# Kernel optimization log

Measured on AMD Instinct MI355X. Metric: run time of the kernel, lower is better.

The kernel has to match this reference:

```python
import jax, jax.numpy as jnp
import numpy as np

EPS = 1e-5

def _layernorm(x, w, b):
    mu = jnp.mean(x, axis=-1, keepdims=True)
    var = jnp.mean(jnp.square(x - mu), axis=-1, keepdims=True)
    return (x - mu) * jax.lax.rsqrt(var + EPS) * w + b

def setup_inputs() -> dict:
    key = jax.random.key(0)
    ks = jax.random.split(key, 8)
    B, N, D = 1, 512, 128
    x = jax.random.normal(ks[0], (B, N, N, D), dtype=jnp.float32)
    mask = jnp.ones((B, N, N), dtype=jnp.float32)
    # learned params (torch nn.Linear stores weight as (out, in))
    p_in_w = jax.random.normal(ks[1], (2 * D, D), dtype=jnp.float32) * (1.0 / np.sqrt(D))
    g_in_w = jax.random.normal(ks[2], (2 * D, D), dtype=jnp.float32) * 0.02
    p_out_w = jax.random.normal(ks[3], (D, D), dtype=jnp.float32) * 0.02
    g_out_w = jax.random.normal(ks[4], (D, D), dtype=jnp.float32) * 0.02
    norm_in_w = jnp.ones((D,), dtype=jnp.float32)
    norm_in_b = jnp.zeros((D,), dtype=jnp.float32)
    norm_out_w = jnp.ones((D,), dtype=jnp.float32)
    norm_out_b = jnp.zeros((D,), dtype=jnp.float32)
    return {"x": x, "mask": mask, "norm_in_w": norm_in_w, "norm_in_b": norm_in_b,
            "p_in_w": p_in_w, "g_in_w": g_in_w, "norm_out_w": norm_out_w,
            "norm_out_b": norm_out_b, "p_out_w": p_out_w, "g_out_w": g_out_w}

def reference(x, mask, norm_in_w, norm_in_b, p_in_w, g_in_w, norm_out_w, norm_out_b, p_out_w, g_out_w):
    # x: (B,N,N,D), mask: (B,N,N)
    x_ln = _layernorm(x, norm_in_w, norm_in_b)          # (B,N,N,D)
    x_in = x_ln
    # gated dual projection to 2D channels, then mask
    h = jnp.einsum('bijd,ed->bije', x_ln, p_in_w) * jax.nn.sigmoid(
        jnp.einsum('bijd,ed->bije', x_ln, g_in_w))      # (B,N,N,2D)
    h = h * mask[..., None]
    D = x.shape[-1]
    a, b = h[..., :D], h[..., D:]                        # (B,N,N,D) each
    # triangular 'outgoing' contraction over k
    t = jnp.einsum('bikd,bjkd->bijd', a, b)              # (B,N,N,D)
    out = jnp.einsum('bijd,ed->bije', _layernorm(t, norm_out_w, norm_out_b), p_out_w) \
        * jax.nn.sigmoid(jnp.einsum('bijd,ed->bije', x_in, g_out_w))
    return out
```

## Files before the change

kernel.cpp:

```cpp
#include <hip/hip_runtime.h>
#include <stdint.h>

#define NSEQ 512
#define DDIM 128
#define NROWS (NSEQ * NSEQ)
#define PMASK (NROWS - 1)
#define ROT(idx, d) (((idx) + (d) * 128) & PMASK)

typedef __bf16 bf16x8 __attribute__((ext_vector_type(8)));
typedef __bf16 bf16x2v __attribute__((ext_vector_type(2)));
typedef unsigned short u16;
typedef u16 ushort8 __attribute__((ext_vector_type(8)));
typedef float f32x4 __attribute__((ext_vector_type(4)));
typedef uint32_t u32x4 __attribute__((ext_vector_type(4)));
typedef uint32_t u32x2 __attribute__((ext_vector_type(2)));

__device__ __forceinline__ u16 cvt1(float f) {
  return __builtin_bit_cast(u16, (__bf16)f);
}
__device__ __forceinline__ uint32_t pk2(float a, float b) {
  bf16x2v v = {(__bf16)a, (__bf16)b};
  return __builtin_bit_cast(uint32_t, v);
}
__device__ __forceinline__ float bf2f(u16 u) {
  uint32_t x = ((uint32_t)u) << 16;
  return __builtin_bit_cast(float, x);
}
__device__ __forceinline__ f32x4 mfma_bf16(ushort8 a, ushort8 b, f32x4 c) {
  return __builtin_amdgcn_mfma_f32_16x16x32_bf16(
      __builtin_bit_cast(bf16x8, a), __builtin_bit_cast(bf16x8, b), c, 0, 0, 0);
}
__device__ __forceinline__ float sigmoidf_(float x) {
  return __builtin_amdgcn_rcpf(1.0f + __expf(-x));
}

#define ROR16(v, n)                                                            \
  __builtin_bit_cast(float, __builtin_amdgcn_update_dpp(                       \
      __builtin_bit_cast(int, (v)), __builtin_bit_cast(int, (v)),              \
      0x120 + (n), 0xF, 0xF, false))

#define GLOAD16(gp, lp)                                                        \
  __builtin_amdgcn_global_load_lds(                                            \
      (const __attribute__((address_space(1))) void*)(gp),                     \
      (__attribute__((address_space(3))) void*)(lp), 16, 0, 0)

__global__ __launch_bounds__(256) void k0_prep(
    const float* __restrict__ p_in_w, const float* __restrict__ g_in_w,
    const float* __restrict__ p_out_w, const float* __restrict__ g_out_w,
    const float* __restrict__ now, const float* __restrict__ nob,
    u16* __restrict__ Wb, u16* __restrict__ Pb, u16* __restrict__ Gb,
    float* __restrict__ S12) {
  const int b = blockIdx.x, t = threadIdx.x;
#pragma unroll
  for (int k = 0; k < 2; ++k) {
    const int idx = b * 512 + k * 256 + t;
    const float v = (idx < 32768) ? p_in_w[idx] : g_in_w[idx - 32768];
    Wb[idx] = cvt1(v);
  }
  if (t < 128) {
    const int idx = b * 128 + t;
    const int d = idx & 127;
    Pb[idx] = cvt1(p_out_w[idx] * now[d]);
    Gb[idx] = cvt1(g_out_w[idx]);
  }
  const int w = t >> 6, lane = t & 63;
  if (w >= 2) {
    const float* wv = (w == 2) ? now : nob;
    float p = p_out_w[b * 128 + lane] * wv[lane] +
              p_out_w[b * 128 + 64 + lane] * wv[64 + lane];
#pragma unroll
    for (int m = 1; m < 64; m <<= 1) p += __shfl_xor(p, m);
    if (lane == 0) S12[2 * b + (w - 2)] = p;
  }
}

__global__ __launch_bounds__(256, 6) void k1_ln_proj(
    const float* __restrict__ x, const float* __restrict__ mask,
    const float* __restrict__ niw, const float* __restrict__ nib,
    const u16* __restrict__ Wb, const u16* __restrict__ Gb,
    u16* __restrict__ AtB, u16* __restrict__ gArg) {
  __shared__ __align__(16) u16 xln[64 * 128];
  __shared__ __align__(16) u16 stage[64 * 64];
  const int tid = threadIdx.x;
  const int lane = tid & 63;
  const int w = tid >> 6;
  const int bid = blockIdx.x;
  const int rb = (bid >> 5) * 8 + (bid & 7);
  const int cg = (bid >> 3) & 3;
  const int r0 = rb * 64;
  const int g = lane >> 4, c = lane & 15;

  f32x4 v0[4], v1[4];
#pragma unroll
  for (int it = 0; it < 4; ++it) {
    const int rl = w * 16 + it * 4 + g;
    const float* xr = x + (size_t)(r0 + rl) * DDIM + c * 8;
    v0[it] = *(const f32x4*)xr;
    v1[it] = *(const f32x4*)(xr + 4);
  }
  const f32x4 w0 = *(const f32x4*)(niw + c * 8);
  const f32x4 w1 = *(const f32x4*)(niw + c * 8 + 4);
  const f32x4 b0 = *(const f32x4*)(nib + c * 8);
  const f32x4 b1 = *(const f32x4*)(nib + c * 8 + 4);
#pragma unroll
  for (int it = 0; it < 4; ++it) {
    const int rl = w * 16 + it * 4 + g;
    float s = v0[it][0] + v0[it][1] + v0[it][2] + v0[it][3] +
              v1[it][0] + v1[it][1] + v1[it][2] + v1[it][3];
    float ss = v0[it][0] * v0[it][0] + v0[it][1] * v0[it][1] +
               v0[it][2] * v0[it][2] + v0[it][3] * v0[it][3] +
               v1[it][0] * v1[it][0] + v1[it][1] * v1[it][1] +
               v1[it][2] * v1[it][2] + v1[it][3] * v1[it][3];
    { float t1 = ROR16(s, 1); s += t1; t1 = ROR16(ss, 1); ss += t1; }
    { float t1 = ROR16(s, 2); s += t1; t1 = ROR16(ss, 2); ss += t1; }
    { float t1 = ROR16(s, 4); s += t1; t1 = ROR16(ss, 4); ss += t1; }
    { float t1 = ROR16(s, 8); s += t1; t1 = ROR16(ss, 8); ss += t1; }
    const float mu = s * (1.0f / 128.0f);
    const float rs = rsqrtf(ss * (1.0f / 128.0f) - mu * mu + 1e-5f);
    float f0 = (v0[it][0] - mu) * rs * w0[0] + b0[0];
    float f1 = (v0[it][1] - mu) * rs * w0[1] + b0[1];
    float f2 = (v0[it][2] - mu) * rs * w0[2] + b0[2];
    float f3 = (v0[it][3] - mu) * rs * w0[3] + b0[3];
    float f4 = (v1[it][0] - mu) * rs * w1[0] + b1[0];
    float f5 = (v1[it][1] - mu) * rs * w1[1] + b1[1];
    float f6 = (v1[it][2] - mu) * rs * w1[2] + b1[2];
    float f7 = (v1[it][3] - mu) * rs * w1[3] + b1[3];
    u32x4 ov{pk2(f0, f1), pk2(f2, f3), pk2(f4, f5), pk2(f6, f7)};
    const int byteoff = rl * 256 + ((c ^ (rl & 7)) << 4);
    *(u32x4*)((char*)xln + byteoff) = ov;
  }
  __syncthreads();

  const int lr = lane & 15, lq = lane >> 4;
  const int eP = cg * 64 + w * 16;
  f32x4 accP[4], accG[4];
#pragma unroll
  for (int m = 0; m < 4; ++m) {
    accP[m] = f32x4{0.f, 0.f, 0.f, 0.f};
    accG[m] = f32x4{0.f, 0.f, 0.f, 0.f};
  }

#pragma unroll
  for (int ks = 0; ks < 4; ++ks) {
    const int kblk = ks * 4 + lq;
    ushort8 af[4];
#pragma unroll
    for (int m = 0; m < 4; ++m) {
      const int row = m * 16 + lr;
      af[m] = *(const ushort8*)((const char*)xln + row * 256 +
                                ((kblk ^ (row & 7)) << 4));
    }
    const int e = eP + lr;
    const int dd = ks * 32 + lq * 8;
    const ushort8 bP = *(const ushort8*)(Wb + e * 128 + dd);
    const ushort8 bG = *(const ushort8*)(Wb + (256 + e) * 128 + dd);
#pragma unroll
    for (int m = 0; m < 4; ++m) {
      accP[m] = mfma_bf16(af[m], bP, accP[m]);
      accG[m] = mfma_bf16(af[m], bG, accG[m]);
    }
  }

  const int dloc = w * 16 + lr;
#pragma unroll
  for (int m = 0; m < 4; ++m) {
    const int rloc = m * 16 + lq * 4;
    const f32x4 mv = *(const f32x4*)(mask + r0 + rloc);
    const float o0 = accP[m][0] * sigmoidf_(accG[m][0]) * mv[0];
    const float o1 = accP[m][1] * sigmoidf_(accG[m][1]) * mv[1];
    const float o2 = accP[m][2] * sigmoidf_(accG[m][2]) * mv[2];
    const float o3 = accP[m][3] * sigmoidf_(accG[m][3]) * mv[3];
    u32x2 pk;
    pk[0] = pk2(o0, o1);
    pk[1] = pk2(o2, o3);
    const int gsw = (m * 4 + lq) ^ (dloc & 15);
    *(u32x2*)((char*)stage + dloc * 128 + (gsw << 3)) = pk;
  }
  __syncthreads();

  {
    const int i_ = rb >> 3, kt = rb & 7;
    u16* dst = AtB + (((size_t)kt * 512 + i_) * 256 + cg * 64) * 64;
#pragma unroll
    for (int q = 0; q < 2; ++q) {
      const int e = q * 32 + (tid >> 3);
      const int g0 = (tid & 7) * 2;
      const u32x2 lo =
          *(const u32x2*)((const char*)stage + e * 128 + ((g0 ^ (e & 15)) << 3));
      const u32x2 hi = *(const u32x2*)((const char*)stage + e * 128 +
                                       (((g0 + 1) ^ (e & 15)) << 3));
      u32x4 outv{lo[0], lo[1], hi[0], hi[1]};
      *(u32x4*)(dst + e * 64 + (tid & 7) * 8) = outv;
    }
  }

  if (cg < 2) {
    f32x4 accO[4];
#pragma unroll
    for (int m = 0; m < 4; ++m) accO[m] = f32x4{0.f, 0.f, 0.f, 0.f};
    const int eg = cg * 64 + w * 16 + lr;
#pragma unroll
    for (int ks = 0; ks < 4; ++ks) {
      const int kblk = ks * 4 + lq;
      const ushort8 bO = *(const ushort8*)(Gb + eg * 128 + ks * 32 + lq * 8);
#pragma unroll
      for (int m = 0; m < 4; ++m) {
        const int row = m * 16 + lr;
        const ushort8 af2 = *(const ushort8*)((const char*)xln + row * 256 +
                                              ((kblk ^ (row & 7)) << 4));
        accO[m] = mfma_bf16(af2, bO, accO[m]);
      }
    }
    __syncthreads();
    u16* stage2 = stage;
    const int e_loc = w * 16 + lr;
    const int gsl = e_loc >> 2;
    const int esub = (e_loc & 3) * 2;
#pragma unroll
    for (int m = 0; m < 4; ++m) {
#pragma unroll
      for (int reg = 0; reg < 4; ++reg) {
        const int rl2 = m * 16 + lq * 4 + reg;
        *(u16*)((char*)stage2 + rl2 * 128 + ((gsl ^ (rl2 & 7)) << 3) + esub) =
            cvt1(accO[m][reg]);
      }
    }
    __syncthreads();
#pragma unroll
    for (int p = 0; p < 2; ++p) {
      const int r = p * 32 + (tid >> 3);
      const int il8 = tid & 7;
      const char* base = (const char*)stage2 + r * 128;
      const u32x2 a = *(const u32x2*)(base + (((il8 * 2) ^ (r & 7)) << 3));
      const u32x2 b = *(const u32x2*)(base + (((il8 * 2 + 1) ^ (r & 7)) << 3));
      u32x4 ov{a[0], a[1], b[0], b[1]};
      *(u32x4*)(gArg + (size_t)(r0 + r) * DDIM + cg * 64 + il8 * 8) = ov;
    }
  }
}

__global__ __launch_bounds__(256, 4) void k2_tri(const u16* __restrict__ AtB,
                                                 u16* __restrict__ Ct) {
  __shared__ __align__(16) u16 lds[16384];
  const int tid = threadIdx.x;
  const int bid = blockIdx.x;
  const int lb = (bid & 7) * 256 + (bid >> 3);
  const int d = lb >> 4;
  const int tile = lb & 15;
  const int i0 = (tile >> 2) * 128, j0 = (tile & 3) * 128;
  const int lane = tid & 63, wid = tid >> 6;
  const int wr = wid >> 1, wc = wid & 1;
  const int lr = lane & 15, lq = lane >> 4;

  f32x4 acc[4][4];
#pragma unroll
  for (int m = 0; m < 4; ++m)
#pragma unroll
    for (int n = 0; n < 4; ++n) acc[m][n] = f32x4{0.f, 0.f, 0.f, 0.f};

  for (int kt = 0; kt < 8; ++kt) {
    if (kt) __syncthreads();
#pragma unroll
    for (int q = 0; q < 4; ++q) {
      const int idx = q * 256 + tid;
      const int r = idx >> 3, bk = idx & 7;
      const int sbk = bk ^ (r & 7);
      GLOAD16(AtB + (((size_t)kt * 512 + i0 + r) * 256 + d) * 64 + sbk * 8,
              &lds[idx * 8]);
      GLOAD16(AtB + (((size_t)kt * 512 + j0 + r) * 256 + 128 + d) * 64 + sbk * 8,
              &lds[8192 + idx * 8]);
    }
    __syncthreads();

    const u16* A_l = lds;
    const u16* B_l = lds + 8192;
#pragma unroll
    for (int ks = 0; ks < 2; ++ks) {
      const int kblk = ks * 4 + lq;
      ushort8 af[4], bfr[4];
#pragma unroll
      for (int m = 0; m < 4; ++m) {
        const int row = wr * 64 + m * 16 + lr;
        af[m] = *(const ushort8*)((const char*)A_l + row * 128 +
                                  ((kblk ^ (row & 7)) << 4));
      }
#pragma unroll
      for (int n = 0; n < 4; ++n) {
        const int col = wc * 64 + n * 16 + lr;
        bfr[n] = *(const ushort8*)((const char*)B_l + col * 128 +
                                   ((kblk ^ (col & 7)) << 4));
      }
#pragma unroll
      for (int m = 0; m < 4; ++m)
#pragma unroll
        for (int n = 0; n < 4; ++n)
          acc[m][n] = mfma_bf16(af[m], bfr[n], acc[m][n]);
    }
  }

  u16* Cd = Ct + (size_t)d * NROWS;
#pragma unroll
  for (int m = 0; m < 4; ++m) {
    const int i = i0 + wr * 64 + m * 16 + lq * 4;
#pragma unroll
    for (int n = 0; n < 4; ++n) {
      const int j = j0 + wc * 64 + n * 16 + lr;
#pragma unroll
      for (int reg = 0; reg < 4; ++reg)
        Cd[ROT((i + reg) * NSEQ + j, d)] = cvt1(acc[m][n][reg]);
    }
  }
}

__global__ __launch_bounds__(256, 4) void k3_out(
    const u16* __restrict__ Ct, const u16* __restrict__ gArg,
    const u16* __restrict__ Pb, const float* __restrict__ S12,
    float* __restrict__ out) {
  __shared__ __align__(16) u16 ldsT[128 * 128];
  __shared__ float ps[4 * 128], pss[4 * 128];
  __shared__ float prm[128 * 2];
  __shared__ float s12l[128 * 2];
  const int tid = threadIdx.x, lane = tid & 63, w = tid >> 6;
  const int c0 = blockIdx.x * 128;

  {
    const int row2 = lane * 2;
    float s0 = 0.f, ss0 = 0.f, s1 = 0.f, ss1 = 0.f;
#pragma unroll
    for (int db = 0; db < 4; ++db) {
      uint32_t pe[4], po[4];
#pragma unroll
      for (int j = 0; j < 8; ++j) {
        const int d = w * 32 + db * 8 + j;
        const uint32_t v = *(const uint32_t*)(Ct + (size_t)d * NROWS +
                                              ROT(c0 + row2, d));
        const u16 ue = (u16)v, uo = (u16)(v >> 16);
        const float fe = bf2f(ue), fo = bf2f(uo);
        s0 += fe; ss0 += fe * fe;
        s1 += fo; ss1 += fo * fo;
        if (j & 1) {
          pe[j >> 1] |= ((uint32_t)ue) << 16;
          po[j >> 1] |= ((uint32_t)uo) << 16;
        } else {
          pe[j >> 1] = ue;
          po[j >> 1] = uo;
        }
      }
      const int gr = w * 4 + db;
      *(u32x4*)((char*)ldsT + row2 * 256 + ((gr ^ (row2 & 7)) << 4)) =
          u32x4{pe[0], pe[1], pe[2], pe[3]};
      *(u32x4*)((char*)ldsT + (row2 + 1) * 256 + ((gr ^ ((row2 + 1) & 7)) << 4)) =
          u32x4{po[0], po[1], po[2], po[3]};
    }
    ps[w * 128 + row2] = s0;
    pss[w * 128 + row2] = ss0;
    ps[w * 128 + row2 + 1] = s1;
    pss[w * 128 + row2 + 1] = ss1;
  }
  if (tid < 128) ((u32x2*)s12l)[tid] = ((const u32x2*)S12)[tid];
  __syncthreads();
  if (tid < 128) {
    const float s = ps[tid] + ps[128 + tid] + ps[256 + tid] + ps[384 + tid];
    const float ss = pss[tid] + pss[128 + tid] + pss[256 + tid] + pss[384 + tid];
    const float mu = s * (1.f / 128.f);
    const float rs = rsqrtf(ss * (1.f / 128.f) - mu * mu + 1e-5f);
    prm[2 * tid] = rs;
    prm[2 * tid + 1] = -rs * mu;
  }

  const int lr = lane & 15, lq = lane >> 4;
  const int rowbase = w * 32;
  f32x4 aP[2][8];
#pragma unroll
  for (int m = 0; m < 2; ++m)
#pragma unroll
    for (int n = 0; n < 8; ++n) aP[m][n] = f32x4{0.f, 0.f, 0.f, 0.f};
#pragma unroll
  for (int ks = 0; ks < 4; ++ks) {
    const int kblk = ks * 4 + lq;
    ushort8 at2[2];
#pragma unroll
    for (int m = 0; m < 2; ++m) {
      const int row = rowbase + m * 16 + lr;
      at2[m] = *(const ushort8*)((const char*)ldsT + row * 256 +
                                 ((kblk ^ (row & 7)) << 4));
    }
    ushort8 bp[8];
#pragma unroll
    for (int n = 0; n < 8; ++n) {
      const int e = n * 16 + lr;
      bp[n] = *(const ushort8*)(Pb + e * 128 + ks * 32 + lq * 8);
    }
#pragma unroll
    for (int m = 0; m < 2; ++m)
#pragma unroll
      for (int n = 0; n < 8; ++n) aP[m][n] = mfma_bf16(at2[m], bp[n], aP[m][n]);
  }
  __syncthreads();

#pragma unroll
  for (int m = 0; m < 2; ++m) {
    const int crow = rowbase + m * 16 + lq * 4;
#pragma unroll
    for (int n = 0; n < 8; ++n) {
      const int e = n * 16 + lr;
      const float s1 = s12l[2 * e], s2v = s12l[2 * e + 1];
#pragma unroll
      for (int reg = 0; reg < 4; ++reg) {
        const float rs = prm[2 * (crow + reg)];
        const float t1 = prm[2 * (crow + reg) + 1];
        const float op = rs * aP[m][n][reg] + t1 * s1 + s2v;
        const size_t r = (size_t)(c0 + crow + reg);
        const float gt = sigmoidf_(bf2f(gArg[r * DDIM + e]));
        out[r * DDIM + e] = op * gt;
      }
    }
  }
}

extern "C" void kernel_launch(void* const* d_in, const int* in_sizes, int n_in,
                              void* d_out, int out_size, void* d_ws,
                              size_t ws_size, hipStream_t stream) {
  const float* x = (const float*)d_in[0];
  const float* mask = (const float*)d_in[1];
  const float* niw = (const float*)d_in[2];
  const float* nib = (const float*)d_in[3];
  const float* p_in_w = (const float*)d_in[4];
  const float* g_in_w = (const float*)d_in[5];
  const float* now = (const float*)d_in[6];
  const float* nob = (const float*)d_in[7];
  const float* p_out_w = (const float*)d_in[8];
  const float* g_out_w = (const float*)d_in[9];
  float* out = (float*)d_out;
  char* ws = (char*)d_ws;

  u16* AtB = (u16*)(ws);
  u16* Ct = (u16*)(ws + 134217728);
  u16* gA = (u16*)(ws + 201326592);
  u16* Wb = (u16*)(ws + 268435456);
  u16* Pb = (u16*)(ws + 268566528);
  u16* Gb = (u16*)(ws + 268599296);
  float* S12 = (float*)(ws + 268632064);

  hipLaunchKernelGGL(k0_prep, dim3(128), dim3(256), 0, stream, p_in_w, g_in_w,
                     p_out_w, g_out_w, now, nob, Wb, Pb, Gb, S12);
  hipLaunchKernelGGL(k1_ln_proj, dim3(4 * NROWS / 64), dim3(256), 0, stream, x,
                     mask, niw, nib, Wb, Gb, AtB, gA);
  hipLaunchKernelGGL(k2_tri, dim3(128 * 16), dim3(256), 0, stream, AtB, Ct);
  hipLaunchKernelGGL(k3_out, dim3(NROWS / 128), dim3(256), 0, stream, Ct, gA,
                     Pb, S12, out);
}
```

Baseline: 322.1 us.

## Make LN-projection blocks loop over four row tiles with register prefetch

The layernorm and input-projection kernel now launches a quarter as many blocks. Each block processes four 64-row tiles in sequence, keeping the same channel group and XCD mapping. While the MFMA projections and stores for the current tile run, the next tile's x rows are loaded into registers, so global-load latency overlaps with compute. The cost is more live registers per thread and less parallelism from independent blocks, and correctness now depends on the barrier placement that guards the reused LDS buffers.

```diff
diff --git a/kernel.cpp b/kernel.cpp
--- a/kernel.cpp
+++ b/kernel.cpp
@@ -85,156 +85,176 @@
   const int lane = tid & 63;
   const int w = tid >> 6;
   const int bid = blockIdx.x;
-  const int rb = (bid >> 5) * 8 + (bid & 7);
+  const int xcd = bid & 7;
   const int cg = (bid >> 3) & 3;
-  const int r0 = rb * 64;
+  const int ub = bid >> 5;
   const int g = lane >> 4, c = lane & 15;
-
-  f32x4 v0[4], v1[4];
-#pragma unroll
-  for (int it = 0; it < 4; ++it) {
-    const int rl = w * 16 + it * 4 + g;
-    const float* xr = x + (size_t)(r0 + rl) * DDIM + c * 8;
-    v0[it] = *(const f32x4*)xr;
-    v1[it] = *(const f32x4*)(xr + 4);
-  }
+  const int lr = lane & 15, lq = lane >> 4;
+
   const f32x4 w0 = *(const f32x4*)(niw + c * 8);
   const f32x4 w1 = *(const f32x4*)(niw + c * 8 + 4);
   const f32x4 b0 = *(const f32x4*)(nib + c * 8);
   const f32x4 b1 = *(const f32x4*)(nib + c * 8 + 4);
-#pragma unroll
+
+  f32x4 v0[4], v1[4];
+  {
+    const int r0n = ((ub * 4 + 0) * 8 + xcd) * 64;
+#pragma unroll
+    for (int itl = 0; itl < 4; ++itl) {
+      const int rl = w * 16 + itl * 4 + g;
+      const float* xr = x + (size_t)(r0n + rl) * DDIM + c * 8;
+      v0[itl] = *(const f32x4*)xr;
+      v1[itl] = *(const f32x4*)(xr + 4);
+    }
+  }
+
   for (int it = 0; it < 4; ++it) {
-    const int rl = w * 16 + it * 4 + g;
-    float s = v0[it][0] + v0[it][1] + v0[it][2] + v0[it][3] +
-              v1[it][0] + v1[it][1] + v1[it][2] + v1[it][3];
-    float ss = v0[it][0] * v0[it][0] + v0[it][1] * v0[it][1] +
-               v0[it][2] * v0[it][2] + v0[it][3] * v0[it][3] +
-               v1[it][0] * v1[it][0] + v1[it][1] * v1[it][1] +
-               v1[it][2] * v1[it][2] + v1[it][3] * v1[it][3];
-    { float t1 = ROR16(s, 1); s += t1; t1 = ROR16(ss, 1); ss += t1; }
-    { float t1 = ROR16(s, 2); s += t1; t1 = ROR16(ss, 2); ss += t1; }
-    { float t1 = ROR16(s, 4); s += t1; t1 = ROR16(ss, 4); ss += t1; }
-    { float t1 = ROR16(s, 8); s += t1; t1 = ROR16(ss, 8); ss += t1; }
-    const float mu = s * (1.0f / 128.0f);
-    const float rs = rsqrtf(ss * (1.0f / 128.0f) - mu * mu + 1e-5f);
-    float f0 = (v0[it][0] - mu) * rs * w0[0] + b0[0];
-    float f1 = (v0[it][1] - mu) * rs * w0[1] + b0[1];
-    float f2 = (v0[it][2] - mu) * rs * w0[2] + b0[2];
-    float f3 = (v0[it][3] - mu) * rs * w0[3] + b0[3];
-    float f4 = (v1[it][0] - mu) * rs * w1[0] + b1[0];
-    float f5 = (v1[it][1] - mu) * rs * w1[1] + b1[1];
-    float f6 = (v1[it][2] - mu) * rs * w1[2] + b1[2];
-    float f7 = (v1[it][3] - mu) * rs * w1[3] + b1[3];
-    u32x4 ov{pk2(f0, f1), pk2(f2, f3), pk2(f4, f5), pk2(f6, f7)};
-    const int byteoff = rl * 256 + ((c ^ (rl & 7)) << 4);
-    *(u32x4*)((char*)xln + byteoff) = ov;
-  }
-  __syncthreads();
-
-  const int lr = lane & 15, lq = lane >> 4;
-  const int eP = cg * 64 + w * 16;
-  f32x4 accP[4], accG[4];
-#pragma unroll
-  for (int m = 0; m < 4; ++m) {
-    accP[m] = f32x4{0.f, 0.f, 0.f, 0.f};
-    accG[m] = f32x4{0.f, 0.f, 0.f, 0.f};
-  }
-
-#pragma unroll
-  for (int ks = 0; ks < 4; ++ks) {
-    const int kblk = ks * 4 + lq;
-    ushort8 af[4];
+    const int rb = (ub * 4 + it) * 8 + xcd;
+    const int r0 = rb * 64;
+
+#pragma unroll
+    for (int itl = 0; itl < 4; ++itl) {
+      const int rl = w * 16 + itl * 4 + g;
+      float s = v0[itl][0] + v0[itl][1] + v0[itl][2] + v0[itl][3] +
+                v1[itl][0] + v1[itl][1] + v1[itl][2] + v1[itl][3];
+      float ss = v0[itl][0] * v0[itl][0] + v0[itl][1] * v0[itl][1] +
+                 v0[itl][2] * v0[itl][2] + v0[itl][3] * v0[itl][3] +
+                 v1[itl][0] * v1[itl][0] + v1[itl][1] * v1[itl][1] +
+                 v1[itl][2] * v1[itl][2] + v1[itl][3] * v1[itl][3];
+      { float t1 = ROR16(s, 1); s += t1; t1 = ROR16(ss, 1); ss += t1; }
+      { float t1 = ROR16(s, 2); s += t1; t1 = ROR16(ss, 2); ss += t1; }
+      { float t1 = ROR16(s, 4); s += t1; t1 = ROR16(ss, 4); ss += t1; }
+      { float t1 = ROR16(s, 8); s += t1; t1 = ROR16(ss, 8); ss += t1; }
+      const float mu = s * (1.0f / 128.0f);
+      const float rs = rsqrtf(ss * (1.0f / 128.0f) - mu * mu + 1e-5f);
+      const float f0 = (v0[itl][0] - mu) * rs * w0[0] + b0[0];
+      const float f1 = (v0[itl][1] - mu) * rs * w0[1] + b0[1];
+      const float f2 = (v0[itl][2] - mu) * rs * w0[2] + b0[2];
+      const float f3 = (v0[itl][3] - mu) * rs * w0[3] + b0[3];
+      const float f4 = (v1[itl][0] - mu) * rs * w1[0] + b1[0];
+      const float f5 = (v1[itl][1] - mu) * rs * w1[1] + b1[1];
+      const float f6 = (v1[itl][2] - mu) * rs * w1[2] + b1[2];
+      const float f7 = (v1[itl][3] - mu) * rs * w1[3] + b1[3];
+      u32x4 ov{pk2(f0, f1), pk2(f2, f3), pk2(f4, f5), pk2(f6, f7)};
+      const int byteoff = rl * 256 + ((c ^ (rl & 7)) << 4);
+      *(u32x4*)((char*)xln + byteoff) = ov;
+    }
+    __syncthreads();
+
+    if (it < 3) {
+      const int r0n = ((ub * 4 + it + 1) * 8 + xcd) * 64;
+#pragma unroll
+      for (int itl = 0; itl < 4; ++itl) {
+        const int rl = w * 16 + itl * 4 + g;
+        const float* xr = x + (size_t)(r0n + rl) * DDIM + c * 8;
+        v0[itl] = *(const f32x4*)xr;
+        v1[itl] = *(const f32x4*)(xr + 4);
+      }
+    }
+
+    const int eP = cg * 64 + w * 16;
+    f32x4 accP[4], accG[4];
 #pragma unroll
     for (int m = 0; m < 4; ++m) {
-      const int row = m * 16 + lr;
-      af[m] = *(const ushort8*)((const char*)xln + row * 256 +
-                                ((kblk ^ (row & 7)) << 4));
-    }
-    const int e = eP + lr;
-    const int dd = ks * 32 + lq * 8;
-    const ushort8 bP = *(const ushort8*)(Wb + e * 128 + dd);
-    const ushort8 bG = *(const ushort8*)(Wb + (256 + e) * 128 + dd);
-#pragma unroll
-    for (int m = 0; m < 4; ++m) {
-      accP[m] = mfma_bf16(af[m], bP, accP[m]);
-      accG[m] = mfma_bf16(af[m], bG, accG[m]);
-    }
-  }
-
-  const int dloc = w * 16 + lr;
-#pragma unroll
-  for (int m = 0; m < 4; ++m) {
-    const int rloc = m * 16 + lq * 4;
-    const f32x4 mv = *(const f32x4*)(mask + r0 + rloc);
-    const float o0 = accP[m][0] * sigmoidf_(accG[m][0]) * mv[0];
-    const float o1 = accP[m][1] * sigmoidf_(accG[m][1]) * mv[1];
-    const float o2 = accP[m][2] * sigmoidf_(accG[m][2]) * mv[2];
-    const float o3 = accP[m][3] * sigmoidf_(accG[m][3]) * mv[3];
-    u32x2 pk;
-    pk[0] = pk2(o0, o1);
-    pk[1] = pk2(o2, o3);
-    const int gsw = (m * 4 + lq) ^ (dloc & 15);
-    *(u32x2*)((char*)stage + dloc * 128 + (gsw << 3)) = pk;
-  }
-  __syncthreads();
-
-  {
-    const int i_ = rb >> 3, kt = rb & 7;
-    u16* dst = AtB + (((size_t)kt * 512 + i_) * 256 + cg * 64) * 64;
-#pragma unroll
-    for (int q = 0; q < 2; ++q) {
-      const int e = q * 32 + (tid >> 3);
-      const int g0 = (tid & 7) * 2;
-      const u32x2 lo =
-          *(const u32x2*)((const char*)stage + e * 128 + ((g0 ^ (e & 15)) << 3));
-      const u32x2 hi = *(const u32x2*)((const char*)stage + e * 128 +
-                                       (((g0 + 1) ^ (e & 15)) << 3));
-      u32x4 outv{lo[0], lo[1], hi[0], hi[1]};
-      *(u32x4*)(dst + e * 64 + (tid & 7) * 8) = outv;
-    }
-  }
-
-  if (cg < 2) {
-    f32x4 accO[4];
-#pragma unroll
-    for (int m = 0; m < 4; ++m) accO[m] = f32x4{0.f, 0.f, 0.f, 0.f};
-    const int eg = cg * 64 + w * 16 + lr;
+      accP[m] = f32x4{0.f, 0.f, 0.f, 0.f};
+      accG[m] = f32x4{0.f, 0.f, 0.f, 0.f};
+    }
 #pragma unroll
     for (int ks = 0; ks < 4; ++ks) {
       const int kblk = ks * 4 + lq;
-      const ushort8 bO = *(const ushort8*)(Gb + eg * 128 + ks * 32 + lq * 8);
+      ushort8 af[4];
 #pragma unroll
       for (int m = 0; m < 4; ++m) {
         const int row = m * 16 + lr;
-        const ushort8 af2 = *(const ushort8*)((const char*)xln + row * 256 +
-                                              ((kblk ^ (row & 7)) << 4));
-        accO[m] = mfma_bf16(af2, bO, accO[m]);
-      }
+        af[m] = *(const ushort8*)((const char*)xln + row * 256 +
+                                  ((kblk ^ (row & 7)) << 4));
+      }
+      const int e = eP + lr;
+      const int dd = ks * 32 + lq * 8;
+      const ushort8 bP = *(const ushort8*)(Wb + e * 128 + dd);
+      const ushort8 bG = *(const ushort8*)(Wb + (256 + e) * 128 + dd);
+#pragma unroll
+      for (int m = 0; m < 4; ++m) {
+        accP[m] = mfma_bf16(af[m], bP, accP[m]);
+        accG[m] = mfma_bf16(af[m], bG, accG[m]);
+      }
+    }
+
+    const int dloc = w * 16 + lr;
+#pragma unroll
+    for (int m = 0; m < 4; ++m) {
+      const int rloc = m * 16 + lq * 4;
+      const f32x4 mv = *(const f32x4*)(mask + r0 + rloc);
+      const float o0 = accP[m][0] * sigmoidf_(accG[m][0]) * mv[0];
+      const float o1 = accP[m][1] * sigmoidf_(accG[m][1]) * mv[1];
+      const float o2 = accP[m][2] * sigmoidf_(accG[m][2]) * mv[2];
+      const float o3 = accP[m][3] * sigmoidf_(accG[m][3]) * mv[3];
+      u32x2 pk;
+      pk[0] = pk2(o0, o1);
+      pk[1] = pk2(o2, o3);
+      const int gsw = (m * 4 + lq) ^ (dloc & 15);
+      *(u32x2*)((char*)stage + dloc * 128 + (gsw << 3)) = pk;
     }
     __syncthreads();
-    u16* stage2 = stage;
-    const int e_loc = w * 16 + lr;
-    const int gsl = e_loc >> 2;
-    const int esub = (e_loc & 3) * 2;
-#pragma unroll
-    for (int m = 0; m < 4; ++m) {
-#pragma unroll
-      for (int reg = 0; reg < 4; ++reg) {
-        const int rl2 = m * 16 + lq * 4 + reg;
-        *(u16*)((char*)stage2 + rl2 * 128 + ((gsl ^ (rl2 & 7)) << 3) + esub) =
-            cvt1(accO[m][reg]);
-      }
-    }
-    __syncthreads();
-#pragma unroll
-    for (int p = 0; p < 2; ++p) {
-      const int r = p * 32 + (tid >> 3);
-      const int il8 = tid & 7;
-      const char* base = (const char*)stage2 + r * 128;
-      const u32x2 a = *(const u32x2*)(base + (((il8 * 2) ^ (r & 7)) << 3));
-      const u32x2 b = *(const u32x2*)(base + (((il8 * 2 + 1) ^ (r & 7)) << 3));
-      u32x4 ov{a[0], a[1], b[0], b[1]};
-      *(u32x4*)(gArg + (size_t)(r0 + r) * DDIM + cg * 64 + il8 * 8) = ov;
+
+    {
+      const int i_ = rb >> 3, kt = rb & 7;
+      u16* dst = AtB + (((size_t)kt * 512 + i_) * 256 + cg * 64) * 64;
+#pragma unroll
+      for (int q = 0; q < 2; ++q) {
+        const int e = q * 32 + (tid >> 3);
+        const int g0 = (tid & 7) * 2;
+        const u32x2 lo = *(const u32x2*)((const char*)stage + e * 128 +
+                                         ((g0 ^ (e & 15)) << 3));
+        const u32x2 hi = *(const u32x2*)((const char*)stage + e * 128 +
+                                         (((g0 + 1) ^ (e & 15)) << 3));
+        u32x4 outv{lo[0], lo[1], hi[0], hi[1]};
+        *(u32x4*)(dst + e * 64 + (tid & 7) * 8) = outv;
+      }
+    }
+
+    if (cg < 2) {
+      f32x4 accO[4];
+#pragma unroll
+      for (int m = 0; m < 4; ++m) accO[m] = f32x4{0.f, 0.f, 0.f, 0.f};
+      const int eg = cg * 64 + w * 16 + lr;
+#pragma unroll
+      for (int ks = 0; ks < 4; ++ks) {
+        const int kblk = ks * 4 + lq;
+        const ushort8 bO = *(const ushort8*)(Gb + eg * 128 + ks * 32 + lq * 8);
+#pragma unroll
+        for (int m = 0; m < 4; ++m) {
+          const int row = m * 16 + lr;
+          const ushort8 af2 = *(const ushort8*)((const char*)xln + row * 256 +
+                                                ((kblk ^ (row & 7)) << 4));
+          accO[m] = mfma_bf16(af2, bO, accO[m]);
+        }
+      }
+      __syncthreads();
+      u16* stage2 = stage;
+      const int e_loc = w * 16 + lr;
+      const int gsl = e_loc >> 2;
+      const int esub = (e_loc & 3) * 2;
+#pragma unroll
+      for (int m = 0; m < 4; ++m) {
+#pragma unroll
+        for (int reg = 0; reg < 4; ++reg) {
+          const int rl2 = m * 16 + lq * 4 + reg;
+          *(u16*)((char*)stage2 + rl2 * 128 + ((gsl ^ (rl2 & 7)) << 3) + esub) =
+              cvt1(accO[m][reg]);
+        }
+      }
+      __syncthreads();
+#pragma unroll
+      for (int p = 0; p < 2; ++p) {
+        const int r = p * 32 + (tid >> 3);
+        const int il8 = tid & 7;
+        const char* base = (const char*)stage2 + r * 128;
+        const u32x2 a = *(const u32x2*)(base + (((il8 * 2) ^ (r & 7)) << 3));
+        const u32x2 b = *(const u32x2*)(base + (((il8 * 2 + 1) ^ (r & 7)) << 3));
+        u32x4 ov{a[0], a[1], b[0], b[1]};
+        *(u32x4*)(gArg + (size_t)(r0 + r) * DDIM + cg * 64 + il8 * 8) = ov;
+      }
     }
   }
 }
@@ -444,8 +464,8 @@
 
   hipLaunchKernelGGL(k0_prep, dim3(128), dim3(256), 0, stream, p_in_w, g_in_w,
                      p_out_w, g_out_w, now, nob, Wb, Pb, Gb, S12);
-  hipLaunchKernelGGL(k1_ln_proj, dim3(4 * NROWS / 64), dim3(256), 0, stream, x,
-                     mask, niw, nib, Wb, Gb, AtB, gA);
+  hipLaunchKernelGGL(k1_ln_proj, dim3(4096), dim3(256), 0, stream, x, mask,
+                     niw, nib, Wb, Gb, AtB, gA);
   hipLaunchKernelGGL(k2_tri, dim3(128 * 16), dim3(256), 0, stream, AtB, Ct);
   hipLaunchKernelGGL(k3_out, dim3(NROWS / 128), dim3(256), 0, stream, Ct, gA,
                      Pb, S12, out);
```

New measurement: 637.5 us. 98.0% more time.

## Halve k1 column groups so each block computes 128 output channels

Applied to the files above, without the earlier changes.

The LN+projection kernel now splits the 256 gated channels across 2 column groups instead of 4, with each wave computing two 16-wide channel tiles. Each 64-row tile of x is therefore loaded and layer-normalized twice instead of four times, cutting redundant global reads and LN work. The gate-out projection now runs in every block. The cost is more accumulator registers and a larger staging buffer, so launch bounds drop to 4 blocks per SM and occupancy may fall.

```diff
diff --git a/kernel.cpp b/kernel.cpp
--- a/kernel.cpp
+++ b/kernel.cpp
@@ -74,19 +74,19 @@
   }
 }
 
-__global__ __launch_bounds__(256, 6) void k1_ln_proj(
+__global__ __launch_bounds__(256, 4) void k1_ln_proj(
     const float* __restrict__ x, const float* __restrict__ mask,
     const float* __restrict__ niw, const float* __restrict__ nib,
     const u16* __restrict__ Wb, const u16* __restrict__ Gb,
     u16* __restrict__ AtB, u16* __restrict__ gArg) {
   __shared__ __align__(16) u16 xln[64 * 128];
-  __shared__ __align__(16) u16 stage[64 * 64];
+  __shared__ __align__(16) u16 stage[128 * 64];
   const int tid = threadIdx.x;
   const int lane = tid & 63;
   const int w = tid >> 6;
   const int bid = blockIdx.x;
-  const int rb = (bid >> 5) * 8 + (bid & 7);
-  const int cg = (bid >> 3) & 3;
+  const int rb = (bid >> 4) * 8 + (bid & 7);
+  const int cg = (bid >> 3) & 1;
   const int r0 = rb * 64;
   const int g = lane >> 4, c = lane & 15;
 
@@ -132,14 +132,15 @@
   __syncthreads();
 
   const int lr = lane & 15, lq = lane >> 4;
-  const int eP = cg * 64 + w * 16;
-  f32x4 accP[4], accG[4];
-#pragma unroll
-  for (int m = 0; m < 4; ++m) {
-    accP[m] = f32x4{0.f, 0.f, 0.f, 0.f};
-    accG[m] = f32x4{0.f, 0.f, 0.f, 0.f};
-  }
-
+  const int eP = cg * 128 + w * 32;
+  f32x4 accP[4][2], accG[4][2];
+#pragma unroll
+  for (int m = 0; m < 4; ++m)
+#pragma unroll
+    for (int n = 0; n < 2; ++n) {
+      accP[m][n] = f32x4{0.f, 0.f, 0.f, 0.f};
+      accG[m][n] = f32x4{0.f, 0.f, 0.f, 0.f};
+    }
 #pragma unroll
   for (int ks = 0; ks < 4; ++ks) {
     const int kblk = ks * 4 + lq;
@@ -150,39 +151,48 @@
       af[m] = *(const ushort8*)((const char*)xln + row * 256 +
                                 ((kblk ^ (row & 7)) << 4));
     }
-    const int e = eP + lr;
-    const int dd = ks * 32 + lq * 8;
-    const ushort8 bP = *(const ushort8*)(Wb + e * 128 + dd);
-    const ushort8 bG = *(const ushort8*)(Wb + (256 + e) * 128 + dd);
-#pragma unroll
-    for (int m = 0; m < 4; ++m) {
-      accP[m] = mfma_bf16(af[m], bP, accP[m]);
-      accG[m] = mfma_bf16(af[m], bG, accG[m]);
-    }
-  }
-
-  const int dloc = w * 16 + lr;
+    ushort8 bP[2], bG[2];
+#pragma unroll
+    for (int n = 0; n < 2; ++n) {
+      const int e = eP + n * 16 + lr;
+      const int dd = ks * 32 + lq * 8;
+      bP[n] = *(const ushort8*)(Wb + e * 128 + dd);
+      bG[n] = *(const ushort8*)(Wb + (256 + e) * 128 + dd);
+    }
+#pragma unroll
+    for (int m = 0; m < 4; ++m)
+#pragma unroll
+      for (int n = 0; n < 2; ++n) {
+        accP[m][n] = mfma_bf16(af[m], bP[n], accP[m][n]);
+        accG[m][n] = mfma_bf16(af[m], bG[n], accG[m][n]);
+      }
+  }
+
 #pragma unroll
   for (int m = 0; m < 4; ++m) {
     const int rloc = m * 16 + lq * 4;
     const f32x4 mv = *(const f32x4*)(mask + r0 + rloc);
-    const float o0 = accP[m][0] * sigmoidf_(accG[m][0]) * mv[0];
-    const float o1 = accP[m][1] * sigmoidf_(accG[m][1]) * mv[1];
-    const float o2 = accP[m][2] * sigmoidf_(accG[m][2]) * mv[2];
-    const float o3 = accP[m][3] * sigmoidf_(accG[m][3]) * mv[3];
-    u32x2 pk;
-    pk[0] = pk2(o0, o1);
-    pk[1] = pk2(o2, o3);
-    const int gsw = (m * 4 + lq) ^ (dloc & 15);
-    *(u32x2*)((char*)stage + dloc * 128 + (gsw << 3)) = pk;
+#pragma unroll
+    for (int n = 0; n < 2; ++n) {
+      const int dloc = w * 32 + n * 16 + lr;
+      const float o0 = accP[m][n][0] * sigmoidf_(accG[m][n][0]) * mv[0];
+      const float o1 = accP[m][n][1] * sigmoidf_(accG[m][n][1]) * mv[1];
+      const float o2 = accP[m][n][2] * sigmoidf_(accG[m][n][2]) * mv[2];
+      const float o3 = accP[m][n][3] * sigmoidf_(accG[m][n][3]) * mv[3];
+      u32x2 pk;
+      pk[0] = pk2(o0, o1);
+      pk[1] = pk2(o2, o3);
+      const int gsw = (m * 4 + lq) ^ (dloc & 15);
+      *(u32x2*)((char*)stage + dloc * 128 + (gsw << 3)) = pk;
+    }
   }
   __syncthreads();
 
   {
     const int i_ = rb >> 3, kt = rb & 7;
-    u16* dst = AtB + (((size_t)kt * 512 + i_) * 256 + cg * 64) * 64;
-#pragma unroll
-    for (int q = 0; q < 2; ++q) {
+    u16* dst = AtB + (((size_t)kt * 512 + i_) * 256 + cg * 128) * 64;
+#pragma unroll
+    for (int q = 0; q < 4; ++q) {
       const int e = q * 32 + (tid >> 3);
       const int g0 = (tid & 7) * 2;
       const u32x2 lo =
@@ -194,7 +204,7 @@
     }
   }
 
-  if (cg < 2) {
+  {
     f32x4 accO[4];
 #pragma unroll
     for (int m = 0; m < 4; ++m) accO[m] = f32x4{0.f, 0.f, 0.f, 0.f};
@@ -444,7 +454,7 @@
 
   hipLaunchKernelGGL(k0_prep, dim3(128), dim3(256), 0, stream, p_in_w, g_in_w,
                      p_out_w, g_out_w, now, nob, Wb, Pb, Gb, S12);
-  hipLaunchKernelGGL(k1_ln_proj, dim3(4 * NROWS / 64), dim3(256), 0, stream, x,
+  hipLaunchKernelGGL(k1_ln_proj, dim3(2 * NROWS / 64), dim3(256), 0, stream, x,
                      mask, niw, nib, Wb, Gb, AtB, gA);
   hipLaunchKernelGGL(k2_tri, dim3(128 * 16), dim3(256), 0, stream, AtB, Ct);
   hipLaunchKernelGGL(k3_out, dim3(NROWS / 128), dim3(256), 0, stream, Ct, gA,
```

Measured after the change: 311.6 us. 1.03x faster.
